# Kernel tuning notes

Hardware: AMD Instinct MI355X
Metric: run time of the kernel (lower is better)

Reference implementation:

```python
import jax, jax.numpy as jnp
import numpy as np

N_BATCH = 50000   # nodes being aggregated (rows of mask)
N_UNIQUE = 100000 # unique neighbor nodes (cols of mask / rows of features)
K = 16            # sampled neighbors per node
HID = 256
POOL = 128


def setup_inputs() -> dict:
    key = jax.random.key(0)
    k1, k2, k3 = jax.random.split(key, 3)
    neigh_idx = jax.random.randint(k1, (N_BATCH, K), 0, N_UNIQUE, dtype=jnp.int64)
    features = jax.random.normal(k2, (N_UNIQUE, HID), dtype=jnp.float32)
    # pool_layer weight, nn.Linear(hid, pool, bias=False): shape [pool, hid]
    W = jax.random.normal(k3, (POOL, HID), dtype=jnp.float32) * (1.0 / np.sqrt(HID))
    return {"neigh_idx": neigh_idx, "features": features, "W": W}


def reference(neigh_idx, features, W):
    # pool_feats = pool_layer(features): [M, POOL]
    pool_feats = jnp.einsum("mh,ph->mp", features, W)
    # mean over sampled neighbors, equivalent to (mask / num_neigh) @ pool_feats
    # without materializing the dense [N, M] mask.
    to_feats = jnp.mean(pool_feats[neigh_idx], axis=1)  # [N, POOL]
    return to_feats
```

## Files before the change

kernel.cpp:

```cpp
#include <hip/hip_runtime.h>


#define N_NODES  50000
#define N_UNIQUE 100000
#define KNEI     16
#define HID      256
#define POOL     128

#define NBLOCKS  512
#define NPB      ((N_NODES + NBLOCKS - 1) / NBLOCKS)

__global__ __launch_bounds__(256) void fused_meanpool_kernel(
    const int*   __restrict__ idx,
    const float* __restrict__ feats,
    const float* __restrict__ W,
    float* __restrict__ out)
{
    __shared__ float  mf[HID];
    __shared__ float4 part[8][32];

    const int tid = threadIdx.x;
    const int og  = tid & 31;
    const int ksl = tid >> 5;

    float4 w[4][8];
#pragma unroll
    for (int e = 0; e < 4; ++e) {
        const float* wr = W + (size_t)(og * 4 + e) * HID + ksl * 32;
#pragma unroll
        for (int j4 = 0; j4 < 8; ++j4)
            w[e][j4] = *reinterpret_cast<const float4*>(wr + j4 * 4);
    }

    const int node0 = blockIdx.x * NPB;
    for (int i = 0; i < NPB; ++i) {
        const int node = node0 + i;
        if (node >= N_NODES) break;

        const int* ip = idx + node * KNEI;
        float v = 0.f;
#pragma unroll
        for (int k = 0; k < KNEI; ++k) {
            int r = ip[k];
            r = ((unsigned)r < (unsigned)N_UNIQUE) ? r : 0;
            v += feats[(size_t)r * HID + tid];
        }
        mf[tid] = v;
        __syncthreads();

        float4 acc = make_float4(0.f, 0.f, 0.f, 0.f);
        const float4* mfp = reinterpret_cast<const float4*>(&mf[ksl * 32]);
#pragma unroll
        for (int j4 = 0; j4 < 8; ++j4) {
            const float4 m4 = mfp[j4];
            acc.x = fmaf(w[0][j4].x, m4.x, acc.x);
            acc.x = fmaf(w[0][j4].y, m4.y, acc.x);
            acc.x = fmaf(w[0][j4].z, m4.z, acc.x);
            acc.x = fmaf(w[0][j4].w, m4.w, acc.x);
            acc.y = fmaf(w[1][j4].x, m4.x, acc.y);
            acc.y = fmaf(w[1][j4].y, m4.y, acc.y);
            acc.y = fmaf(w[1][j4].z, m4.z, acc.y);
            acc.y = fmaf(w[1][j4].w, m4.w, acc.y);
            acc.z = fmaf(w[2][j4].x, m4.x, acc.z);
            acc.z = fmaf(w[2][j4].y, m4.y, acc.z);
            acc.z = fmaf(w[2][j4].z, m4.z, acc.z);
            acc.z = fmaf(w[2][j4].w, m4.w, acc.z);
            acc.w = fmaf(w[3][j4].x, m4.x, acc.w);
            acc.w = fmaf(w[3][j4].y, m4.y, acc.w);
            acc.w = fmaf(w[3][j4].z, m4.z, acc.w);
            acc.w = fmaf(w[3][j4].w, m4.w, acc.w);
        }
        part[ksl][og] = acc;
        __syncthreads();

        if (tid < 32) {
            float4 s = part[0][tid];
#pragma unroll
            for (int k = 1; k < 8; ++k) {
                const float4 p4 = part[k][tid];
                s.x += p4.x; s.y += p4.y; s.z += p4.z; s.w += p4.w;
            }
            const float inv = 1.f / (float)KNEI;
            s.x *= inv; s.y *= inv; s.z *= inv; s.w *= inv;
            *reinterpret_cast<float4*>(out + (size_t)node * POOL + tid * 4) = s;
        }
    }
}

extern "C" void kernel_launch(void* const* d_in, const int* in_sizes, int n_in,
                              void* d_out, int out_size, void* d_ws, size_t ws_size,
                              hipStream_t stream) {
    const int*   idx   = (const int*)d_in[0];
    const float* feats = (const float*)d_in[1];
    const float* W     = (const float*)d_in[2];
    float* out = (float*)d_out;

    fused_meanpool_kernel<<<NBLOCKS, 256, 0, stream>>>(idx, feats, W, out);
}
```

Before: 287.6 us.

## Project all feature rows first, then gather bf16 pooled rows for mean

Replaces the fused gather-then-project kernel with three kernels: a transpose of W, a tiled fp32 GEMM that projects all unique feature rows to POOL width and stores them as bf16, and a gather kernel that averages 16 projected rows per node. This cuts gather traffic from 256-float rows to 128-bf16 rows. In exchange it adds a full projection pass over all 100k rows and bf16 rounding error in the intermediate.

```diff
diff --git a/kernel.cpp b/kernel.cpp
--- a/kernel.cpp
+++ b/kernel.cpp
@@ -1,90 +1,124 @@
 #include <hip/hip_runtime.h>
 
 
+#define M_ROWS   100000
 #define N_NODES  50000
-#define N_UNIQUE 100000
 #define KNEI     16
 #define HID      256
 #define POOL     128
 
-#define NBLOCKS  512
-#define NPB      ((N_NODES + NBLOCKS - 1) / NBLOCKS)
+__device__ inline unsigned short f32_to_bf16(float f) {
+    union { float f; unsigned u; } v; v.f = f;
+    unsigned r = v.u + 0x7FFFu + ((v.u >> 16) & 1u);
+    return (unsigned short)(r >> 16);
+}
+__device__ inline float bf16_to_f32(unsigned u16) {
+    union { unsigned u; float f; } v; v.u = u16 << 16;
+    return v.f;
+}
 
-__global__ __launch_bounds__(256) void fused_meanpool_kernel(
-    const int*   __restrict__ idx,
-    const float* __restrict__ feats,
-    const float* __restrict__ W,
+__global__ __launch_bounds__(256) void transpose_W_kernel(
+    const float* __restrict__ W, float* __restrict__ Wt)
+{
+    int t = blockIdx.x * 256 + threadIdx.x;
+    if (t < POOL * HID) {
+        int h = t >> 7, p = t & 127;
+        Wt[t] = W[p * HID + h];
+    }
+}
+
+__global__ __launch_bounds__(256) void pool_gemm_kernel(
+    const float* __restrict__ A,
+    const float* __restrict__ Wt,
+    unsigned short* __restrict__ Pb)
+{
+    __shared__ float As[32][132];
+    __shared__ float Bs[32][128];
+    const int tid = threadIdx.x;
+    const int tx = tid & 15;
+    const int ty = tid >> 4;
+    const int bm = blockIdx.x * 128;
+
+    float acc[8][8];
+#pragma unroll
+    for (int i = 0; i < 8; ++i)
+#pragma unroll
+        for (int j = 0; j < 8; ++j) acc[i][j] = 0.f;
+
+    for (int k0 = 0; k0 < HID; k0 += 32) {
+#pragma unroll
+        for (int i = 0; i < 4; ++i) {
+            int f4 = tid + i * 256;
+            int row = f4 >> 3, kk = (f4 & 7) << 2;
+            int gr = bm + row;
+            int grc = (gr < M_ROWS) ? gr : (M_ROWS - 1);
+            float4 v = *reinterpret_cast<const float4*>(A + (size_t)grc * HID + k0 + kk);
+            As[kk + 0][row] = v.x;
+            As[kk + 1][row] = v.y;
+            As[kk + 2][row] = v.z;
+            As[kk + 3][row] = v.w;
+        }
+#pragma unroll
+        for (int i = 0; i < 4; ++i) {
+            int f4 = tid + i * 256;
+            int kk = f4 >> 5, p4 = f4 & 31;
+            float4 v = *reinterpret_cast<const float4*>(Wt + (size_t)(k0 + kk) * POOL + p4 * 4);
+            *reinterpret_cast<float4*>(&Bs[kk][p4 * 4]) = v;
+        }
+        __syncthreads();
+
+#pragma unroll
+        for (int kk = 0; kk < 32; ++kk) {
+            float a[8], b[8];
+            *reinterpret_cast<float4*>(&a[0]) = *reinterpret_cast<const float4*>(&As[kk][ty * 8]);
+            *reinterpret_cast<float4*>(&a[4]) = *reinterpret_cast<const float4*>(&As[kk][ty * 8 + 4]);
+            *reinterpret_cast<float4*>(&b[0]) = *reinterpret_cast<const float4*>(&Bs[kk][tx * 8]);
+            *reinterpret_cast<float4*>(&b[4]) = *reinterpret_cast<const float4*>(&Bs[kk][tx * 8 + 4]);
+#pragma unroll
+            for (int i = 0; i < 8; ++i)
+#pragma unroll
+                for (int j = 0; j < 8; ++j)
+                    acc[i][j] = fmaf(a[i], b[j], acc[i][j]);
+        }
+        __syncthreads();
+    }
+
+#pragma unroll
+    for (int i = 0; i < 8; ++i) {
+        int gr = bm + ty * 8 + i;
+        if (gr < M_ROWS) {
+            uint4 pk;
+            pk.x = (unsigned)f32_to_bf16(acc[i][0]) | ((unsigned)f32_to_bf16(acc[i][1]) << 16);
+            pk.y = (unsigned)f32_to_bf16(acc[i][2]) | ((unsigned)f32_to_bf16(acc[i][3]) << 16);
+            pk.z = (unsigned)f32_to_bf16(acc[i][4]) | ((unsigned)f32_to_bf16(acc[i][5]) << 16);
+            pk.w = (unsigned)f32_to_bf16(acc[i][6]) | ((unsigned)f32_to_bf16(acc[i][7]) << 16);
+            *reinterpret_cast<uint4*>(Pb + (size_t)gr * POOL + tx * 8) = pk;
+        }
+    }
+}
+
+__global__ __launch_bounds__(256) void gather_mean_kernel(
+    const int* __restrict__ idx,
+    const unsigned short* __restrict__ Pb,
     float* __restrict__ out)
 {
-    __shared__ float  mf[HID];
-    __shared__ float4 part[8][32];
+    const int gw   = (blockIdx.x * 256 + threadIdx.x) >> 6;
+    const int lane = threadIdx.x & 63;
+    if (gw >= N_NODES) return;
 
-    const int tid = threadIdx.x;
-    const int og  = tid & 31;
-    const int ksl = tid >> 5;
-
-    float4 w[4][8];
+    const int* ip = idx + (size_t)gw * KNEI;
+    float sx = 0.f, sy = 0.f;
 #pragma unroll
-    for (int e = 0; e < 4; ++e) {
-        const float* wr = W + (size_t)(og * 4 + e) * HID + ksl * 32;
-#pragma unroll
-        for (int j4 = 0; j4 < 8; ++j4)
-            w[e][j4] = *reinterpret_cast<const float4*>(wr + j4 * 4);
+    for (int k = 0; k < KNEI; ++k) {
+        int r = ip[k];
+        r = ((unsigned)r < (unsigned)M_ROWS) ? r : 0;
+        unsigned v = *reinterpret_cast<const unsigned*>(Pb + (size_t)r * POOL + lane * 2);
+        sx += bf16_to_f32(v & 0xFFFFu);
+        sy += bf16_to_f32(v >> 16);
     }
-
-    const int node0 = blockIdx.x * NPB;
-    for (int i = 0; i < NPB; ++i) {
-        const int node = node0 + i;
-        if (node >= N_NODES) break;
-
-        const int* ip = idx + node * KNEI;
-        float v = 0.f;
-#pragma unroll
-        for (int k = 0; k < KNEI; ++k) {
-            int r = ip[k];
-            r = ((unsigned)r < (unsigned)N_UNIQUE) ? r : 0;
-            v += feats[(size_t)r * HID + tid];
-        }
-        mf[tid] = v;
-        __syncthreads();
-
-        float4 acc = make_float4(0.f, 0.f, 0.f, 0.f);
-        const float4* mfp = reinterpret_cast<const float4*>(&mf[ksl * 32]);
-#pragma unroll
-        for (int j4 = 0; j4 < 8; ++j4) {
-            const float4 m4 = mfp[j4];
-            acc.x = fmaf(w[0][j4].x, m4.x, acc.x);
-            acc.x = fmaf(w[0][j4].y, m4.y, acc.x);
-            acc.x = fmaf(w[0][j4].z, m4.z, acc.x);
-            acc.x = fmaf(w[0][j4].w, m4.w, acc.x);
-            acc.y = fmaf(w[1][j4].x, m4.x, acc.y);
-            acc.y = fmaf(w[1][j4].y, m4.y, acc.y);
-            acc.y = fmaf(w[1][j4].z, m4.z, acc.y);
-            acc.y = fmaf(w[1][j4].w, m4.w, acc.y);
-            acc.z = fmaf(w[2][j4].x, m4.x, acc.z);
-            acc.z = fmaf(w[2][j4].y, m4.y, acc.z);
-            acc.z = fmaf(w[2][j4].z, m4.z, acc.z);
-            acc.z = fmaf(w[2][j4].w, m4.w, acc.z);
-            acc.w = fmaf(w[3][j4].x, m4.x, acc.w);
-            acc.w = fmaf(w[3][j4].y, m4.y, acc.w);
-            acc.w = fmaf(w[3][j4].z, m4.z, acc.w);
-            acc.w = fmaf(w[3][j4].w, m4.w, acc.w);
-        }
-        part[ksl][og] = acc;
-        __syncthreads();
-
-        if (tid < 32) {
-            float4 s = part[0][tid];
-#pragma unroll
-            for (int k = 1; k < 8; ++k) {
-                const float4 p4 = part[k][tid];
-                s.x += p4.x; s.y += p4.y; s.z += p4.z; s.w += p4.w;
-            }
-            const float inv = 1.f / (float)KNEI;
-            s.x *= inv; s.y *= inv; s.z *= inv; s.w *= inv;
-            *reinterpret_cast<float4*>(out + (size_t)node * POOL + tid * 4) = s;
-        }
-    }
+    const float inv = 1.f / (float)KNEI;
+    float2 o = make_float2(sx * inv, sy * inv);
+    *reinterpret_cast<float2*>(out + (size_t)gw * POOL + lane * 2) = o;
 }
 
 extern "C" void kernel_launch(void* const* d_in, const int* in_sizes, int n_in,
@@ -95,5 +129,10 @@
     const float* W     = (const float*)d_in[2];
     float* out = (float*)d_out;
 
-    fused_meanpool_kernel<<<NBLOCKS, 256, 0, stream>>>(idx, feats, W, out);
+    unsigned short* Pb = (unsigned short*)d_ws;
+    float* Wt = (float*)((char*)d_ws + (size_t)M_ROWS * POOL * 2);
+
+    transpose_W_kernel<<<(POOL * HID + 255) / 256, 256, 0, stream>>>(W, Wt);
+    pool_gemm_kernel<<<(M_ROWS + 127) / 128, 256, 0, stream>>>(feats, Wt, Pb);
+    gather_mean_kernel<<<(N_NODES * 64 + 255) / 256, 256, 0, stream>>>(idx, Pb, out);
 }
```

Result: faster. 258.3 us (-10.2%).
